# Kernel tuning notes

Measured on AMD Instinct MI355X. Metric: run time of the kernel, lower is better.

Reference implementation:

```python
import jax, jax.numpy as jnp
import numpy as np

T, H, NH, NKV, HD, E, K, I = 1024, 2048, 16, 4, 128, 16, 2, 768
EPS = 1e-6
THETA = 10000.0


def setup_inputs() -> dict:
    key = jax.random.key(0)
    ks = jax.random.split(key, 8)
    s = 0.02
    return {
        "hidden_states": jax.random.normal(ks[0], (T, H), jnp.float32),
        "positions": jnp.arange(T, dtype=jnp.int32),
        "w_norm1": jnp.ones((H,), jnp.float32),
        "w_norm2": jnp.ones((H,), jnp.float32),
        "w_qkv": jax.random.normal(ks[1], (H, (NH + 2 * NKV) * HD), jnp.float32) * s,
        "w_qnorm": jnp.ones((HD,), jnp.float32),
        "w_knorm": jnp.ones((HD,), jnp.float32),
        "w_o": jax.random.normal(ks[2], (NH * HD, H), jnp.float32) * s,
        "w_router": jax.random.normal(ks[3], (H, E), jnp.float32) * s,
        "w_gate": jax.random.normal(ks[4], (E, H, I), jnp.float32) * s,
        "w_up": jax.random.normal(ks[5], (E, H, I), jnp.float32) * s,
        "w_down": jax.random.normal(ks[6], (E, I, H), jnp.float32) * s,
    }


def rmsnorm(x, w):
    return x * jax.lax.rsqrt(jnp.mean(x * x, axis=-1, keepdims=True) + EPS) * w


def apply_rope(x, positions):
    # NEOX-style rotary, full head_dim. x: [T, n_heads, HD]
    half = HD // 2
    inv_freq = 1.0 / (THETA ** (jnp.arange(half, dtype=jnp.float32) / half))
    ang = positions.astype(jnp.float32)[:, None] * inv_freq  # [T, half]
    cos = jnp.cos(ang)[:, None, :]
    sin = jnp.sin(ang)[:, None, :]
    x1, x2 = x[..., :half], x[..., half:]
    return jnp.concatenate([x1 * cos - x2 * sin, x2 * cos + x1 * sin], axis=-1)


def reference(hidden_states, positions, w_norm1, w_norm2, w_qkv, w_qnorm, w_knorm,
              w_o, w_router, w_gate, w_up, w_down):
    # prepare_attn: residual = x; h = input_layernorm(x)
    residual = hidden_states
    h = rmsnorm(hidden_states, w_norm1)

    # --- attention (bidirectional, GQA, per-head q/k RMSNorm + RoPE) ---
    qkv = h @ w_qkv
    q, k, v = jnp.split(qkv, [NH * HD, NH * HD + NKV * HD], axis=-1)
    q = rmsnorm(q.reshape(T, NH, HD), w_qnorm)
    k = rmsnorm(k.reshape(T, NKV, HD), w_knorm)
    v = v.reshape(T, NKV, HD)
    q = apply_rope(q, positions)
    k = apply_rope(k, positions)
    rep = NH // NKV
    kf = jnp.repeat(k, rep, axis=1)  # [T, NH, HD]
    vf = jnp.repeat(v, rep, axis=1)
    scores = jnp.einsum('tnd,snd->nts', q, kf) * (HD ** -0.5)  # [NH, T, T]
    p = jax.nn.softmax(scores, axis=-1)
    ctx = jnp.einsum('nts,snd->tnd', p, vf).reshape(T, NH * HD)
    attn_out = ctx @ w_o

    # prepare_mlp: residual = residual + attn_out; h = post_attention_layernorm(residual)
    residual = residual + attn_out
    h = rmsnorm(residual, w_norm2)

    # --- sparse MoE: softmax router, top-k renormalize, SwiGLU experts ---
    logits = h @ w_router
    probs = jax.nn.softmax(logits, axis=-1)
    topw, topi = jax.lax.top_k(probs, K)
    topw = topw / jnp.sum(topw, axis=-1, keepdims=True)
    gates = jnp.zeros((T, E), h.dtype).at[jnp.arange(T)[:, None], topi].set(topw)
    g = jnp.einsum('th,ehi->eti', h, w_gate)
    u = jnp.einsum('th,ehi->eti', h, w_up)
    y = jnp.einsum('eti,eih->eth', jax.nn.silu(g) * u, w_down)
    moe_out = jnp.einsum('eth,te->th', y, gates)

    return moe_out, residual
```

## Files before the change

kernel.cpp:

```cpp
#include <hip/hip_runtime.h>

#define T_    1024
#define H_    2048
#define NH_   16
#define NKV_  4
#define HD_   128
#define E_    16
#define I_    768
#define QKVN  3072

typedef __attribute__((ext_vector_type(8))) short  short8;
typedef __attribute__((ext_vector_type(4))) float  f32x4;
typedef unsigned short u16;

#define LDP 40

__device__ inline u16 f2bf(float f) {
  unsigned u = __builtin_bit_cast(unsigned, f);
  return (u16)((u + 0x7fffu + ((u >> 16) & 1u)) >> 16);
}
__device__ inline float bf2f(u16 h) {
  unsigned u = ((unsigned)h) << 16;
  return __builtin_bit_cast(float, u);
}

__device__ inline float blk_sum(float v, float* lds) {
#pragma unroll
  for (int o = 32; o; o >>= 1) v += __shfl_down(v, o);
  int w = threadIdx.x >> 6;
  __syncthreads();
  if ((threadIdx.x & 63) == 0) lds[w] = v;
  __syncthreads();
  float s = lds[0];
  int nw = blockDim.x >> 6;
  for (int i = 1; i < nw; ++i) s += lds[i];
  return s;
}
__device__ inline float blk_max(float v, float* lds) {
#pragma unroll
  for (int o = 32; o; o >>= 1) v = fmaxf(v, __shfl_down(v, o));
  int w = threadIdx.x >> 6;
  __syncthreads();
  if ((threadIdx.x & 63) == 0) lds[w] = v;
  __syncthreads();
  float s = lds[0];
  int nw = blockDim.x >> 6;
  for (int i = 1; i < nw; ++i) s = fmaxf(s, lds[i]);
  return s;
}


struct F8 { float v[8]; };

__device__ inline void wrS(u16* lds, const uint4& r) {
  int row = threadIdx.x >> 2, kg = (threadIdx.x & 3) * 8;
  *(uint4*)(lds + row * LDP + kg) = r;
}
__device__ inline void wrS(u16* lds, const F8& r) {
  int n = threadIdx.x & 127, kh = (threadIdx.x >> 7) * 8;
  uint4 w;
  w.x = (unsigned)f2bf(r.v[0]) | ((unsigned)f2bf(r.v[1]) << 16);
  w.y = (unsigned)f2bf(r.v[2]) | ((unsigned)f2bf(r.v[3]) << 16);
  w.z = (unsigned)f2bf(r.v[4]) | ((unsigned)f2bf(r.v[5]) << 16);
  w.w = (unsigned)f2bf(r.v[6]) | ((unsigned)f2bf(r.v[7]) << 16);
  *(uint4*)(lds + n * LDP + kh) = w;
}

__device__ inline void mma8(const u16* As, const u16* Bs, f32x4 acc[4][2]) {
  const int lane = threadIdx.x & 63, wv = threadIdx.x >> 6;
  const int wr = wv >> 2, wc = wv & 3;
  const int kk = (lane >> 4) * 8, rr = lane & 15;
  short8 aF[4], bF[2];
#pragma unroll
  for (int m = 0; m < 4; ++m)
    aF[m] = *(const short8*)(As + (wr * 64 + m * 16 + rr) * LDP + kk);
#pragma unroll
  for (int n = 0; n < 2; ++n)
    bF[n] = *(const short8*)(Bs + (wc * 32 + n * 16 + rr) * LDP + kk);
#pragma unroll
  for (int m = 0; m < 4; ++m)
#pragma unroll
    for (int n = 0; n < 2; ++n)
      acc[m][n] = __builtin_amdgcn_mfma_f32_16x16x32_bf16(aF[m], bF[n], acc[m][n], 0, 0, 0);
}

#define ZERO_ACC(acc) do { \
  _Pragma("unroll") for (int m_ = 0; m_ < 4; ++m_) \
  _Pragma("unroll") for (int n_ = 0; n_ < 2; ++n_) acc[m_][n_] = (f32x4){0.f,0.f,0.f,0.f}; \
} while (0)

#define EPI_ROW(m, r)  (((threadIdx.x >> 6) >> 2) * 64 + (m)*16 + (((threadIdx.x&63) >> 4) * 4) + (r))
#define EPI_COL(n)     ((((threadIdx.x >> 6) & 3) * 32) + (n)*16 + ((threadIdx.x&63) & 15))

template<int NT, class BT, class LA, class LB>
__device__ inline void pipe(LA la, LB lb, u16* A0, u16* B0, u16* A1, u16* B1,
                            f32x4 acc[4][2]) {
  uint4 a0, a1; BT b0, b1;
  la(a0, 0); lb(b0, 0);
  la(a1, 1); lb(b1, 1);
  wrS(A0, a0); wrS(B0, b0);
  la(a0, 2); lb(b0, 2);
#pragma unroll 1
  for (int kt = 0; kt < NT; kt += 2) {
    __syncthreads();
    wrS(A1, a1); wrS(B1, b1);
    if (kt + 3 < NT) { la(a1, kt + 3); lb(b1, kt + 3); }
    mma8(A0, B0, acc);
    __syncthreads();
    if (kt + 2 < NT) { wrS(A0, a0); wrS(B0, b0); }
    if (kt + 4 < NT) { la(a0, kt + 4); lb(b0, kt + 4); }
    mma8(A1, B1, acc);
  }
}


__global__ __launch_bounds__(256) void k_rms1(const float* x, const float* w, u16* out) {
  __shared__ float lds[4];
  int t = blockIdx.x, tid = threadIdx.x;
  float v[8]; float ss = 0.f;
#pragma unroll
  for (int i = 0; i < 8; ++i) { v[i] = x[(size_t)t * H_ + tid + 256 * i]; ss += v[i] * v[i]; }
  ss = blk_sum(ss, lds);
  float inv = rsqrtf(ss * (1.f / H_) + 1e-6f);
#pragma unroll
  for (int i = 0; i < 8; ++i)
    out[(size_t)t * H_ + tid + 256 * i] = f2bf(v[i] * inv * w[tid + 256 * i]);
}

__global__ __launch_bounds__(256) void k_rms2(const float* x, const float* w,
                                              float* outf, u16* outb) {
  __shared__ float lds[4];
  int t = blockIdx.x, tid = threadIdx.x;
  float v[8]; float ss = 0.f;
#pragma unroll
  for (int i = 0; i < 8; ++i) { v[i] = x[(size_t)t * H_ + tid + 256 * i]; ss += v[i] * v[i]; }
  ss = blk_sum(ss, lds);
  float inv = rsqrtf(ss * (1.f / H_) + 1e-6f);
#pragma unroll
  for (int i = 0; i < 8; ++i) {
    float r = v[i] * inv * w[tid + 256 * i];
    outf[(size_t)t * H_ + tid + 256 * i] = r;
    outb[(size_t)t * H_ + tid + 256 * i] = f2bf(r);
  }
}

__global__ __launch_bounds__(512) void k_qkv(const u16* h1, const float* wqkv, float* qkv) {
  __shared__ __align__(16) u16 A0[128 * LDP], B0[128 * LDP], A1[128 * LDP], B1[128 * LDP];
  int bn = blockIdx.x, bm = blockIdx.y;
  f32x4 acc[4][2]; ZERO_ACC(acc);
  auto la = [&](uint4& r, int kt) {
    int row = threadIdx.x >> 2, kg = (threadIdx.x & 3) * 8;
    r = *(const uint4*)(h1 + (size_t)(bm * 128 + row) * H_ + kt * 32 + kg);
  };
  auto lb = [&](F8& r, int kt) {
    int n = threadIdx.x & 127, kh = (threadIdx.x >> 7) * 8;
    const float* src = wqkv + (size_t)(kt * 32 + kh) * QKVN + bn * 128 + n;
#pragma unroll
    for (int j = 0; j < 8; ++j) r.v[j] = src[(size_t)j * QKVN];
  };
  pipe<H_ / 32, F8>(la, lb, A0, B0, A1, B1, acc);
#pragma unroll
  for (int m = 0; m < 4; ++m)
#pragma unroll
    for (int n = 0; n < 2; ++n) {
      f32x4 a = acc[m][n];
#pragma unroll
      for (int r = 0; r < 4; ++r)
        qkv[(size_t)(bm * 128 + EPI_ROW(m, r)) * QKVN + bn * 128 + EPI_COL(n)] = a[r];
    }
}

__global__ __launch_bounds__(256) void k_qkrope(const float* qkv, const int* pos,
                                                const float* wq, const float* wk,
                                                u16* q, u16* kk, u16* vT) {
  __shared__ float cs[64], sn[64];
  int t = blockIdx.x, tid = threadIdx.x, lane = tid & 63, w = tid >> 6;
  if (tid < 64) {
    float fr = expf(-((float)tid / 64.f) * 9.210340371976184f);
    float ang = (float)pos[t] * fr;
    float s_, c_; sincosf(ang, &s_, &c_);
    cs[tid] = c_; sn[tid] = s_;
  }
  __syncthreads();
  const float* row = qkv + (size_t)t * QKVN;
  for (int h = w; h < NH_; h += 4) {
    float x1 = row[h * 128 + lane], x2 = row[h * 128 + 64 + lane];
    float ss = x1 * x1 + x2 * x2;
#pragma unroll
    for (int o = 32; o; o >>= 1) ss += __shfl_down(ss, o);
    ss = __shfl(ss, 0);
    float inv = rsqrtf(ss * (1.f / HD_) + 1e-6f);
    float n1 = x1 * inv * wq[lane], n2 = x2 * inv * wq[64 + lane];
    float o1 = n1 * cs[lane] - n2 * sn[lane];
    float o2 = n2 * cs[lane] + n1 * sn[lane];
    q[(size_t)t * (NH_ * HD_) + h * 128 + lane] = f2bf(o1);
    q[(size_t)t * (NH_ * HD_) + h * 128 + 64 + lane] = f2bf(o2);
  }
  if (w < NKV_) {
    int h = w;
    float x1 = row[2048 + h * 128 + lane], x2 = row[2048 + h * 128 + 64 + lane];
    float ss = x1 * x1 + x2 * x2;
#pragma unroll
    for (int o = 32; o; o >>= 1) ss += __shfl_down(ss, o);
    ss = __shfl(ss, 0);
    float inv = rsqrtf(ss * (1.f / HD_) + 1e-6f);
    float n1 = x1 * inv * wk[lane], n2 = x2 * inv * wk[64 + lane];
    float o1 = n1 * cs[lane] - n2 * sn[lane];
    float o2 = n2 * cs[lane] + n1 * sn[lane];
    kk[((size_t)h * T_ + t) * HD_ + lane] = f2bf(o1);
    kk[((size_t)h * T_ + t) * HD_ + 64 + lane] = f2bf(o2);
    float v1 = row[2560 + h * 128 + lane], v2 = row[2560 + h * 128 + 64 + lane];
    vT[((size_t)(h * 128 + lane)) * T_ + t] = f2bf(v1);
    vT[((size_t)(h * 128 + 64 + lane)) * T_ + t] = f2bf(v2);
  }
}

__global__ __launch_bounds__(512) void k_scores(const u16* q, const u16* kb, u16* S) {
  __shared__ __align__(16) u16 A0[128 * LDP], B0[128 * LDP], A1[128 * LDP], B1[128 * LDP];
  int h = blockIdx.x, sn = blockIdx.y, qm = blockIdx.z;
  const u16* Aq = q + h * 128;
  const u16* Bk = kb + (size_t)(h >> 2) * T_ * HD_;
  f32x4 acc[4][2]; ZERO_ACC(acc);
  auto la = [&](uint4& r, int kt) {
    int row = threadIdx.x >> 2, kg = (threadIdx.x & 3) * 8;
    r = *(const uint4*)(Aq + (size_t)(qm * 128 + row) * (NH_ * HD_) + kt * 32 + kg);
  };
  auto lb = [&](uint4& r, int kt) {
    int row = threadIdx.x >> 2, kg = (threadIdx.x & 3) * 8;
    r = *(const uint4*)(Bk + (size_t)(sn * 128 + row) * HD_ + kt * 32 + kg);
  };
  pipe<HD_ / 32, uint4>(la, lb, A0, B0, A1, B1, acc);
  const float scale = 0.08838834764831845f;
#pragma unroll
  for (int m = 0; m < 4; ++m)
#pragma unroll
    for (int n = 0; n < 2; ++n) {
      f32x4 a = acc[m][n];
#pragma unroll
      for (int r = 0; r < 4; ++r)
        S[((size_t)h * T_ + qm * 128 + EPI_ROW(m, r)) * T_ + sn * 128 + EPI_COL(n)] =
            f2bf(a[r] * scale);
    }
}

__global__ __launch_bounds__(256) void k_softmax(u16* S) {
  __shared__ float lds[4];
  int t = blockIdx.x, h = blockIdx.y, tid = threadIdx.x;
  u16* rowp = S + ((size_t)h * T_ + t) * T_;
  float x[4];
#pragma unroll
  for (int i = 0; i < 4; ++i) x[i] = bf2f(rowp[tid + 256 * i]);
  float m = fmaxf(fmaxf(x[0], x[1]), fmaxf(x[2], x[3]));
  m = blk_max(m, lds);
  float s = 0.f;
#pragma unroll
  for (int i = 0; i < 4; ++i) { x[i] = __expf(x[i] - m); s += x[i]; }
  s = blk_sum(s, lds);
  float inv = 1.f / s;
#pragma unroll
  for (int i = 0; i < 4; ++i) rowp[tid + 256 * i] = f2bf(x[i] * inv);
}

__global__ __launch_bounds__(512) void k_pv(const u16* P, const u16* vT, u16* ctx) {
  __shared__ __align__(16) u16 A0[128 * LDP], B0[128 * LDP], A1[128 * LDP], B1[128 * LDP];
  int h = blockIdx.x, qm = blockIdx.y;
  const u16* Ap = P + (size_t)h * T_ * T_;
  const u16* Bv = vT + (size_t)(h >> 2) * HD_ * T_;
  f32x4 acc[4][2]; ZERO_ACC(acc);
  auto la = [&](uint4& r, int kt) {
    int row = threadIdx.x >> 2, kg = (threadIdx.x & 3) * 8;
    r = *(const uint4*)(Ap + (size_t)(qm * 128 + row) * T_ + kt * 32 + kg);
  };
  auto lb = [&](uint4& r, int kt) {
    int row = threadIdx.x >> 2, kg = (threadIdx.x & 3) * 8;
    r = *(const uint4*)(Bv + (size_t)row * T_ + kt * 32 + kg);
  };
  pipe<T_ / 32, uint4>(la, lb, A0, B0, A1, B1, acc);
#pragma unroll
  for (int m = 0; m < 4; ++m)
#pragma unroll
    for (int n = 0; n < 2; ++n) {
      f32x4 a = acc[m][n];
#pragma unroll
      for (int r = 0; r < 4; ++r)
        ctx[(size_t)(qm * 128 + EPI_ROW(m, r)) * (NH_ * HD_) + h * 128 + EPI_COL(n)] =
            f2bf(a[r]);
    }
}

__global__ __launch_bounds__(512) void k_wo(const u16* ctx, const float* wo,
                                            const float* hs, float* resid) {
  __shared__ __align__(16) u16 A0[128 * LDP], B0[128 * LDP], A1[128 * LDP], B1[128 * LDP];
  int bn = blockIdx.x, bm = blockIdx.y;
  f32x4 acc[4][2]; ZERO_ACC(acc);
  auto la = [&](uint4& r, int kt) {
    int row = threadIdx.x >> 2, kg = (threadIdx.x & 3) * 8;
    r = *(const uint4*)(ctx + (size_t)(bm * 128 + row) * H_ + kt * 32 + kg);
  };
  auto lb = [&](F8& r, int kt) {
    int n = threadIdx.x & 127, kh = (threadIdx.x >> 7) * 8;
    const float* src = wo + (size_t)(kt * 32 + kh) * H_ + bn * 128 + n;
#pragma unroll
    for (int j = 0; j < 8; ++j) r.v[j] = src[(size_t)j * H_];
  };
  pipe<H_ / 32, F8>(la, lb, A0, B0, A1, B1, acc);
#pragma unroll
  for (int m = 0; m < 4; ++m)
#pragma unroll
    for (int n = 0; n < 2; ++n) {
      f32x4 a = acc[m][n];
#pragma unroll
      for (int r = 0; r < 4; ++r) {
        size_t idx = (size_t)(bm * 128 + EPI_ROW(m, r)) * H_ + bn * 128 + EPI_COL(n);
        resid[idx] = a[r] + hs[idx];
      }
    }
}

__global__ __launch_bounds__(256) void k_router(const float* h2f, const float* wr_,
                                                int* topi, float* topw, int* cnt) {
  __shared__ float xs[H_];
  __shared__ float red[4][16];
  __shared__ float lg[16];
  int t = blockIdx.x, tid = threadIdx.x;
#pragma unroll
  for (int i = 0; i < 8; ++i) xs[tid + 256 * i] = h2f[(size_t)t * H_ + tid + 256 * i];
  __syncthreads();
  int e = tid & 15, p = tid >> 4;
  float s = 0.f;
  int b0 = p * 128;
  for (int i = 0; i < 128; ++i) s += xs[b0 + i] * wr_[(size_t)(b0 + i) * E_ + e];
  s += __shfl_down(s, 32);
  s += __shfl_down(s, 16);
  int lane = tid & 63, w = tid >> 6;
  if (lane < 16) red[w][lane] = s;
  __syncthreads();
  if (tid < 16) lg[tid] = red[0][tid] + red[1][tid] + red[2][tid] + red[3][tid];
  __syncthreads();
  if (tid == 0) {
    float l1 = -1e30f; int e1 = 0;
    for (int i = 0; i < E_; ++i) if (lg[i] > l1) { l1 = lg[i]; e1 = i; }
    float l2 = -1e30f; int e2 = 0;
    for (int i = 0; i < E_; ++i) if (i != e1 && lg[i] > l2) { l2 = lg[i]; e2 = i; }
    float d = __expf(l2 - l1);
    float w1 = 1.f / (1.f + d), w2 = d / (1.f + d);
    topi[2 * t] = e1; topi[2 * t + 1] = e2;
    topw[2 * t] = w1; topw[2 * t + 1] = w2;
    atomicAdd(&cnt[e1], 1);
    atomicAdd(&cnt[e2], 1);
  }
}

__global__ void k_scan(const int* cnt, int* basearr) {
  if (threadIdx.x == 0) {
    int b = 0;
    for (int e = 0; e < E_; ++e) { basearr[e] = b; b += cnt[e]; }
    basearr[E_] = b;
  }
}

__global__ __launch_bounds__(256) void k_assign(const int* topi, const float* topw,
                                                const int* basearr, int* posc,
                                                int* tok, float* wslot) {
  int t = blockIdx.x * 256 + threadIdx.x;
  if (t < T_) {
#pragma unroll
    for (int j = 0; j < 2; ++j) {
      int e = topi[2 * t + j];
      int p = atomicAdd(&posc[e], 1);
      int s = basearr[e] + p;
      tok[s] = t;
      wslot[s] = topw[2 * t + j];
    }
  }
}

__global__ __launch_bounds__(512) void k_gateup(const u16* h2b,
                                                const float* wg, const float* wu,
                                                const int* cnt, const int* basearr, const int* tok,
                                                u16* act) {
  __shared__ __align__(16) u16 A0[128 * LDP], B0[128 * LDP], A1[128 * LDP], B1[128 * LDP];
  __shared__ int gat_s[128];
  int e = blockIdx.x;
  int c = cnt[e];
  int mt = blockIdx.z;
  if (mt * 128 >= c) return;
  int basee = basearr[e];
  int gmax = c - mt * 128;
  int n0 = blockIdx.y * 64;
  int tid = threadIdx.x;
  if (tid < 128) {
    int r = mt * 128 + tid;
    gat_s[tid] = (r < c) ? tok[basee + r] : tok[basee];
  }
  __syncthreads();
  const float* Bg = wg + (size_t)e * H_ * I_;
  const float* Bu = wu + (size_t)e * H_ * I_;
  f32x4 acc[4][2]; ZERO_ACC(acc);
  auto la = [&](uint4& r, int kt) {
    int row = threadIdx.x >> 2, kg = (threadIdx.x & 3) * 8;
    r = *(const uint4*)(h2b + (size_t)gat_s[row] * H_ + kt * 32 + kg);
  };
  auto lb = [&](F8& r, int kt) {
    int cidx = threadIdx.x & 127, kh = (threadIdx.x >> 7) * 8;
    int fn = cidx >> 4;
    const float* base = (fn & 1) ? Bu : Bg;
    int col = n0 + (fn >> 1) * 16 + (cidx & 15);
    const float* src = base + (size_t)(kt * 32 + kh) * I_ + col;
#pragma unroll
    for (int j = 0; j < 8; ++j) r.v[j] = src[(size_t)j * I_];
  };
  pipe<H_ / 32, F8>(la, lb, A0, B0, A1, B1, acc);
  int slot0 = basee + mt * 128;
#pragma unroll
  for (int m = 0; m < 4; ++m) {
#pragma unroll
    for (int r = 0; r < 4; ++r) {
      int row = EPI_ROW(m, r);
      if (row >= gmax) continue;
      int col = n0 + ((threadIdx.x >> 6) & 3) * 16 + ((threadIdx.x & 63) & 15);
      float g = acc[m][0][r], u = acc[m][1][r];
      float sg = g / (1.f + __expf(-g));
      act[(size_t)(slot0 + row) * I_ + col] = f2bf(sg * u);
    }
  }
}

__global__ __launch_bounds__(512) void k_down(const u16* act, const float* wd,
                                              const int* cnt, const int* basearr,
                                              const int* tok, const float* wslot,
                                              float* moe) {
  __shared__ __align__(16) u16 A0[128 * LDP], B0[128 * LDP], A1[128 * LDP], B1[128 * LDP];
  int e = blockIdx.y;
  int c = cnt[e];
  int mt = blockIdx.z;
  if (mt * 128 >= c) return;
  int basee = basearr[e];
  int gmax = c - mt * 128;
  int slot0 = basee + mt * 128;
  int n0 = blockIdx.x * 128;
  const u16* Ap = act + (size_t)slot0 * I_;
  const float* Bp = wd + (size_t)e * I_ * H_;
  f32x4 acc[4][2]; ZERO_ACC(acc);
  auto la = [&](uint4& r, int kt) {
    int row = threadIdx.x >> 2, kg = (threadIdx.x & 3) * 8;
    r = *(const uint4*)(Ap + (size_t)row * I_ + kt * 32 + kg);
  };
  auto lb = [&](F8& r, int kt) {
    int n = threadIdx.x & 127, kh = (threadIdx.x >> 7) * 8;
    const float* src = Bp + (size_t)(kt * 32 + kh) * H_ + n0 + n;
#pragma unroll
    for (int j = 0; j < 8; ++j) r.v[j] = src[(size_t)j * H_];
  };
  pipe<I_ / 32, F8>(la, lb, A0, B0, A1, B1, acc);
#pragma unroll
  for (int m = 0; m < 4; ++m)
#pragma unroll
    for (int n = 0; n < 2; ++n) {
      f32x4 a = acc[m][n];
#pragma unroll
      for (int r = 0; r < 4; ++r) {
        int row = EPI_ROW(m, r);
        if (row >= gmax) continue;
        int col = EPI_COL(n);
        int slot = slot0 + row;
        float wgt = wslot[slot];
        int tk = tok[slot];
        atomicAdd(&moe[(size_t)tk * H_ + n0 + col], a[r] * wgt);
      }
    }
}

extern "C" void kernel_launch(void* const* d_in, const int* in_sizes, int n_in,
                              void* d_out, int out_size, void* d_ws, size_t ws_size,
                              hipStream_t stream) {
  const float* hs    = (const float*)d_in[0];
  const int*   pos   = (const int*)d_in[1];
  const float* wn1   = (const float*)d_in[2];
  const float* wn2   = (const float*)d_in[3];
  const float* wqkv  = (const float*)d_in[4];
  const float* wqn   = (const float*)d_in[5];
  const float* wkn   = (const float*)d_in[6];
  const float* wo    = (const float*)d_in[7];
  const float* wrt   = (const float*)d_in[8];
  const float* wg    = (const float*)d_in[9];
  const float* wu    = (const float*)d_in[10];
  const float* wd    = (const float*)d_in[11];
  float* out = (float*)d_out;
  float* moe_out = out;
  float* resid   = out + (size_t)T_ * H_;

  char* ws = (char*)d_ws;
  size_t off = 0;
  auto alloc = [&](size_t bytes) { size_t r = off; off = (off + bytes + 255) & ~(size_t)255; return r; };
  u16*   h1   = (u16*)  (ws + alloc((size_t)T_ * H_ * 2));
  float* qkv  = (float*)(ws + alloc((size_t)T_ * QKVN * 4));
  u16*   q    = (u16*)  (ws + alloc((size_t)T_ * NH_ * HD_ * 2));
  u16*   kb   = (u16*)  (ws + alloc((size_t)NKV_ * T_ * HD_ * 2));
  u16*   vT   = (u16*)  (ws + alloc((size_t)NKV_ * HD_ * T_ * 2));
  u16*   S    = (u16*)  (ws + alloc((size_t)NH_ * T_ * T_ * 2));
  u16*   ctx  = (u16*)  (ws + alloc((size_t)T_ * NH_ * HD_ * 2));
  float* h2f  = (float*)(ws + alloc((size_t)T_ * H_ * 4));
  u16*   h2b  = (u16*)  (ws + alloc((size_t)T_ * H_ * 2));
  u16*   act  = (u16*)  (ws + alloc((size_t)(2 * T_ + 256) * I_ * 2));
  int*   topi = (int*)  (ws + alloc((size_t)T_ * 2 * 4));
  float* topw = (float*)(ws + alloc((size_t)T_ * 2 * 4));
  int*   cnt  = (int*)  (ws + alloc(32 * 4));
  int*   posc = cnt + 16;
  int*   base = (int*)  (ws + alloc(32 * 4));
  int*   tok  = (int*)  (ws + alloc((size_t)(2 * T_ + 128) * 4));
  float* wsl  = (float*)(ws + alloc((size_t)(2 * T_ + 128) * 4));
  (void)ws_size; (void)in_sizes; (void)n_in; (void)out_size;

  hipMemsetAsync(moe_out, 0, (size_t)T_ * H_ * 4, stream);
  hipMemsetAsync(cnt, 0, 32 * 4, stream);

  k_rms1<<<T_, 256, 0, stream>>>(hs, wn1, h1);
  k_qkv<<<dim3(QKVN / 128, T_ / 128), 512, 0, stream>>>(h1, wqkv, qkv);
  k_qkrope<<<T_, 256, 0, stream>>>(qkv, pos, wqn, wkn, q, kb, vT);
  k_scores<<<dim3(NH_, T_ / 128, T_ / 128), 512, 0, stream>>>(q, kb, S);
  k_softmax<<<dim3(T_, NH_), 256, 0, stream>>>(S);
  k_pv<<<dim3(NH_, T_ / 128), 512, 0, stream>>>(S, vT, ctx);
  k_wo<<<dim3(H_ / 128, T_ / 128), 512, 0, stream>>>(ctx, wo, hs, resid);
  k_rms2<<<T_, 256, 0, stream>>>(resid, wn2, h2f, h2b);
  k_router<<<T_, 256, 0, stream>>>(h2f, wrt, topi, topw, cnt);
  k_scan<<<1, 64, 0, stream>>>(cnt, base);
  k_assign<<<4, 256, 0, stream>>>(topi, topw, base, posc, tok, wsl);
  k_gateup<<<dim3(E_, I_ / 64, T_ / 128), 512, 0, stream>>>(h2b, wg, wu, cnt, base, tok, act);
  k_down<<<dim3(H_ / 128, E_, T_ / 128), 512, 0, stream>>>(act, wd, cnt, base, tok, wsl, moe_out);
}
```

Measured before the change: 353.1 us.

## Shrink GEMM tiles to 128x64 with 4-wave blocks and deeper register prefetch

All MFMA GEMM kernels move from 128x128 tiles with 8 waves to 128x64 tiles with 4 waves, doubling grid sizes, and k_pv gains a head-dim split. The A tile load becomes two uint4 per thread. The pipeline now keeps four k-steps of global loads in registers, up from two. This is meant to raise block count and occupancy for these small GEMMs and hide more load latency, at the cost of more register pressure and lower per-block data reuse (more redundant A-tile reads).

```diff
diff --git a/kernel.cpp b/kernel.cpp
--- a/kernel.cpp
+++ b/kernel.cpp
@@ -50,14 +50,19 @@
 }
 
 
+struct A2 { uint4 x, y; };
 struct F8 { float v[8]; };
 
+__device__ inline void wrS(u16* lds, const A2& r) {
+  int u0 = threadIdx.x, u1 = threadIdx.x + 256;
+  *(uint4*)(lds + (u0 >> 2) * LDP + (u0 & 3) * 8) = r.x;
+  *(uint4*)(lds + (u1 >> 2) * LDP + (u1 & 3) * 8) = r.y;
+}
 __device__ inline void wrS(u16* lds, const uint4& r) {
-  int row = threadIdx.x >> 2, kg = (threadIdx.x & 3) * 8;
-  *(uint4*)(lds + row * LDP + kg) = r;
+  *(uint4*)(lds + (threadIdx.x >> 2) * LDP + (threadIdx.x & 3) * 8) = r;
 }
 __device__ inline void wrS(u16* lds, const F8& r) {
-  int n = threadIdx.x & 127, kh = (threadIdx.x >> 7) * 8;
+  int n = threadIdx.x & 63, kh = (threadIdx.x >> 6) * 8;
   uint4 w;
   w.x = (unsigned)f2bf(r.v[0]) | ((unsigned)f2bf(r.v[1]) << 16);
   w.y = (unsigned)f2bf(r.v[2]) | ((unsigned)f2bf(r.v[3]) << 16);
@@ -66,9 +71,9 @@
   *(uint4*)(lds + n * LDP + kh) = w;
 }
 
-__device__ inline void mma8(const u16* As, const u16* Bs, f32x4 acc[4][2]) {
+__device__ inline void mma4(const u16* As, const u16* Bs, f32x4 acc[4][2]) {
   const int lane = threadIdx.x & 63, wv = threadIdx.x >> 6;
-  const int wr = wv >> 2, wc = wv & 3;
+  const int wr = wv >> 1, wc = wv & 1;
   const int kk = (lane >> 4) * 8, rr = lane & 15;
   short8 aF[4], bF[2];
 #pragma unroll
@@ -89,27 +94,35 @@
   _Pragma("unroll") for (int n_ = 0; n_ < 2; ++n_) acc[m_][n_] = (f32x4){0.f,0.f,0.f,0.f}; \
 } while (0)
 
-#define EPI_ROW(m, r)  (((threadIdx.x >> 6) >> 2) * 64 + (m)*16 + (((threadIdx.x&63) >> 4) * 4) + (r))
-#define EPI_COL(n)     ((((threadIdx.x >> 6) & 3) * 32) + (n)*16 + ((threadIdx.x&63) & 15))
-
-template<int NT, class BT, class LA, class LB>
-__device__ inline void pipe(LA la, LB lb, u16* A0, u16* B0, u16* A1, u16* B1,
-                            f32x4 acc[4][2]) {
-  uint4 a0, a1; BT b0, b1;
-  la(a0, 0); lb(b0, 0);
-  la(a1, 1); lb(b1, 1);
+#define EPI_ROW(m, r)  (((threadIdx.x >> 6) >> 1) * 64 + (m)*16 + (((threadIdx.x&63) >> 4) * 4) + (r))
+#define EPI_COL(n)     ((((threadIdx.x >> 6) & 1) * 32) + (n)*16 + ((threadIdx.x&63) & 15))
+
+template<int NT, class AT, class BT, class LA, class LB>
+__device__ inline void pipe4(LA la, LB lb, u16* A0, u16* B0, u16* A1, u16* B1,
+                             f32x4 acc[4][2]) {
+  AT a0, a1, a2, a3; BT b0, b1, b2, b3;
+  la(a0, 0); lb(b0, 0); la(a1, 1); lb(b1, 1);
+  la(a2, 2); lb(b2, 2); la(a3, 3); lb(b3, 3);
   wrS(A0, a0); wrS(B0, b0);
-  la(a0, 2); lb(b0, 2);
+  if (NT > 4) { la(a0, 4); lb(b0, 4); }
 #pragma unroll 1
-  for (int kt = 0; kt < NT; kt += 2) {
+  for (int kt = 0; kt < NT; kt += 4) {
     __syncthreads();
     wrS(A1, a1); wrS(B1, b1);
-    if (kt + 3 < NT) { la(a1, kt + 3); lb(b1, kt + 3); }
-    mma8(A0, B0, acc);
+    if (kt + 5 < NT) { la(a1, kt + 5); lb(b1, kt + 5); }
+    mma4(A0, B0, acc);
     __syncthreads();
-    if (kt + 2 < NT) { wrS(A0, a0); wrS(B0, b0); }
-    if (kt + 4 < NT) { la(a0, kt + 4); lb(b0, kt + 4); }
-    mma8(A1, B1, acc);
+    wrS(A0, a2); wrS(B0, b2);
+    if (kt + 6 < NT) { la(a2, kt + 6); lb(b2, kt + 6); }
+    mma4(A1, B1, acc);
+    __syncthreads();
+    wrS(A1, a3); wrS(B1, b3);
+    if (kt + 7 < NT) { la(a3, kt + 7); lb(b3, kt + 7); }
+    mma4(A0, B0, acc);
+    __syncthreads();
+    if (kt + 4 < NT) { wrS(A0, a0); wrS(B0, b0); }
+    if (kt + 8 < NT) { la(a0, kt + 8); lb(b0, kt + 8); }
+    mma4(A1, B1, acc);
   }
 }
 
@@ -144,21 +157,22 @@
   }
 }
 
-__global__ __launch_bounds__(512) void k_qkv(const u16* h1, const float* wqkv, float* qkv) {
-  __shared__ __align__(16) u16 A0[128 * LDP], B0[128 * LDP], A1[128 * LDP], B1[128 * LDP];
+__global__ __launch_bounds__(256) void k_qkv(const u16* h1, const float* wqkv, float* qkv) {
+  __shared__ __align__(16) u16 A0[128 * LDP], B0[64 * LDP], A1[128 * LDP], B1[64 * LDP];
   int bn = blockIdx.x, bm = blockIdx.y;
   f32x4 acc[4][2]; ZERO_ACC(acc);
-  auto la = [&](uint4& r, int kt) {
-    int row = threadIdx.x >> 2, kg = (threadIdx.x & 3) * 8;
-    r = *(const uint4*)(h1 + (size_t)(bm * 128 + row) * H_ + kt * 32 + kg);
+  auto la = [&](A2& r, int kt) {
+    int u0 = threadIdx.x, u1 = threadIdx.x + 256;
+    r.x = *(const uint4*)(h1 + (size_t)(bm * 128 + (u0 >> 2)) * H_ + kt * 32 + (u0 & 3) * 8);
+    r.y = *(const uint4*)(h1 + (size_t)(bm * 128 + (u1 >> 2)) * H_ + kt * 32 + (u1 & 3) * 8);
   };
   auto lb = [&](F8& r, int kt) {
-    int n = threadIdx.x & 127, kh = (threadIdx.x >> 7) * 8;
-    const float* src = wqkv + (size_t)(kt * 32 + kh) * QKVN + bn * 128 + n;
+    int n = threadIdx.x & 63, kh = (threadIdx.x >> 6) * 8;
+    const float* src = wqkv + (size_t)(kt * 32 + kh) * QKVN + bn * 64 + n;
 #pragma unroll
     for (int j = 0; j < 8; ++j) r.v[j] = src[(size_t)j * QKVN];
   };
-  pipe<H_ / 32, F8>(la, lb, A0, B0, A1, B1, acc);
+  pipe4<H_ / 32, A2, F8>(la, lb, A0, B0, A1, B1, acc);
 #pragma unroll
   for (int m = 0; m < 4; ++m)
 #pragma unroll
@@ -166,7 +180,7 @@
       f32x4 a = acc[m][n];
 #pragma unroll
       for (int r = 0; r < 4; ++r)
-        qkv[(size_t)(bm * 128 + EPI_ROW(m, r)) * QKVN + bn * 128 + EPI_COL(n)] = a[r];
+        qkv[(size_t)(bm * 128 + EPI_ROW(m, r)) * QKVN + bn * 64 + EPI_COL(n)] = a[r];
     }
 }
 
@@ -215,21 +229,21 @@
   }
 }
 
-__global__ __launch_bounds__(512) void k_scores(const u16* q, const u16* kb, u16* S) {
-  __shared__ __align__(16) u16 A0[128 * LDP], B0[128 * LDP], A1[128 * LDP], B1[128 * LDP];
+__global__ __launch_bounds__(256) void k_scores(const u16* q, const u16* kb, u16* S) {
+  __shared__ __align__(16) u16 A0[128 * LDP], B0[64 * LDP], A1[128 * LDP], B1[64 * LDP];
   int h = blockIdx.x, sn = blockIdx.y, qm = blockIdx.z;
   const u16* Aq = q + h * 128;
   const u16* Bk = kb + (size_t)(h >> 2) * T_ * HD_;
   f32x4 acc[4][2]; ZERO_ACC(acc);
-  auto la = [&](uint4& r, int kt) {
-    int row = threadIdx.x >> 2, kg = (threadIdx.x & 3) * 8;
-    r = *(const uint4*)(Aq + (size_t)(qm * 128 + row) * (NH_ * HD_) + kt * 32 + kg);
+  auto la = [&](A2& r, int kt) {
+    int u0 = threadIdx.x, u1 = threadIdx.x + 256;
+    r.x = *(const uint4*)(Aq + (size_t)(qm * 128 + (u0 >> 2)) * (NH_ * HD_) + kt * 32 + (u0 & 3) * 8);
+    r.y = *(const uint4*)(Aq + (size_t)(qm * 128 + (u1 >> 2)) * (NH_ * HD_) + kt * 32 + (u1 & 3) * 8);
   };
   auto lb = [&](uint4& r, int kt) {
-    int row = threadIdx.x >> 2, kg = (threadIdx.x & 3) * 8;
-    r = *(const uint4*)(Bk + (size_t)(sn * 128 + row) * HD_ + kt * 32 + kg);
-  };
-  pipe<HD_ / 32, uint4>(la, lb, A0, B0, A1, B1, acc);
+    r = *(const uint4*)(Bk + (size_t)(sn * 64 + (threadIdx.x >> 2)) * HD_ + kt * 32 + (threadIdx.x & 3) * 8);
+  };
+  pipe4<HD_ / 32, A2, uint4>(la, lb, A0, B0, A1, B1, acc);
   const float scale = 0.08838834764831845f;
 #pragma unroll
   for (int m = 0; m < 4; ++m)
@@ -238,7 +252,7 @@
       f32x4 a = acc[m][n];
 #pragma unroll
       for (int r = 0; r < 4; ++r)
-        S[((size_t)h * T_ + qm * 128 + EPI_ROW(m, r)) * T_ + sn * 128 + EPI_COL(n)] =
+        S[((size_t)h * T_ + qm * 128 + EPI_ROW(m, r)) * T_ + sn * 64 + EPI_COL(n)] =
             f2bf(a[r] * scale);
     }
 }
@@ -261,21 +275,21 @@
   for (int i = 0; i < 4; ++i) rowp[tid + 256 * i] = f2bf(x[i] * inv);
 }
 
-__global__ __launch_bounds__(512) void k_pv(const u16* P, const u16* vT, u16* ctx) {
-  __shared__ __align__(16) u16 A0[128 * LDP], B0[128 * LDP], A1[128 * LDP], B1[128 * LDP];
-  int h = blockIdx.x, qm = blockIdx.y;
+__global__ __launch_bounds__(256) void k_pv(const u16* P, const u16* vT, u16* ctx) {
+  __shared__ __align__(16) u16 A0[128 * LDP], B0[64 * LDP], A1[128 * LDP], B1[64 * LDP];
+  int h = blockIdx.x, qm = blockIdx.y, nb = blockIdx.z;
   const u16* Ap = P + (size_t)h * T_ * T_;
-  const u16* Bv = vT + (size_t)(h >> 2) * HD_ * T_;
+  const u16* Bv = vT + (size_t)(h >> 2) * HD_ * T_ + (size_t)nb * 64 * T_;
   f32x4 acc[4][2]; ZERO_ACC(acc);
-  auto la = [&](uint4& r, int kt) {
-    int row = threadIdx.x >> 2, kg = (threadIdx.x & 3) * 8;
-    r = *(const uint4*)(Ap + (size_t)(qm * 128 + row) * T_ + kt * 32 + kg);
+  auto la = [&](A2& r, int kt) {
+    int u0 = threadIdx.x, u1 = threadIdx.x + 256;
+    r.x = *(const uint4*)(Ap + (size_t)(qm * 128 + (u0 >> 2)) * T_ + kt * 32 + (u0 & 3) * 8);
+    r.y = *(const uint4*)(Ap + (size_t)(qm * 128 + (u1 >> 2)) * T_ + kt * 32 + (u1 & 3) * 8);
   };
   auto lb = [&](uint4& r, int kt) {
-    int row = threadIdx.x >> 2, kg = (threadIdx.x & 3) * 8;
-    r = *(const uint4*)(Bv + (size_t)row * T_ + kt * 32 + kg);
-  };
-  pipe<T_ / 32, uint4>(la, lb, A0, B0, A1, B1, acc);
+    r = *(const uint4*)(Bv + (size_t)(threadIdx.x >> 2) * T_ + kt * 32 + (threadIdx.x & 3) * 8);
+  };
+  pipe4<T_ / 32, A2, uint4>(la, lb, A0, B0, A1, B1, acc);
 #pragma unroll
   for (int m = 0; m < 4; ++m)
 #pragma unroll
@@ -283,27 +297,28 @@
       f32x4 a = acc[m][n];
 #pragma unroll
       for (int r = 0; r < 4; ++r)
-        ctx[(size_t)(qm * 128 + EPI_ROW(m, r)) * (NH_ * HD_) + h * 128 + EPI_COL(n)] =
+        ctx[(size_t)(qm * 128 + EPI_ROW(m, r)) * (NH_ * HD_) + h * 128 + nb * 64 + EPI_COL(n)] =
             f2bf(a[r]);
     }
 }
 
-__global__ __launch_bounds__(512) void k_wo(const u16* ctx, const float* wo,
+__global__ __launch_bounds__(256) void k_wo(const u16* ctx, const float* wo,
                                             const float* hs, float* resid) {
-  __shared__ __align__(16) u16 A0[128 * LDP], B0[128 * LDP], A1[128 * LDP], B1[128 * LDP];
+  __shared__ __align__(16) u16 A0[128 * LDP], B0[64 * LDP], A1[128 * LDP], B1[64 * LDP];
   int bn = blockIdx.x, bm = blockIdx.y;
   f32x4 acc[4][2]; ZERO_ACC(acc);
-  auto la = [&](uint4& r, int kt) {
-    int row = threadIdx.x >> 2, kg = (threadIdx.x & 3) * 8;
-    r = *(const uint4*)(ctx + (size_t)(bm * 128 + row) * H_ + kt * 32 + kg);
+  auto la = [&](A2& r, int kt) {
+    int u0 = threadIdx.x, u1 = threadIdx.x + 256;
+    r.x = *(const uint4*)(ctx + (size_t)(bm * 128 + (u0 >> 2)) * H_ + kt * 32 + (u0 & 3) * 8);
+    r.y = *(const uint4*)(ctx + (size_t)(bm * 128 + (u1 >> 2)) * H_ + kt * 32 + (u1 & 3) * 8);
   };
   auto lb = [&](F8& r, int kt) {
-    int n = threadIdx.x & 127, kh = (threadIdx.x >> 7) * 8;
-    const float* src = wo + (size_t)(kt * 32 + kh) * H_ + bn * 128 + n;
+    int n = threadIdx.x & 63, kh = (threadIdx.x >> 6) * 8;
+    const float* src = wo + (size_t)(kt * 32 + kh) * H_ + bn * 64 + n;
 #pragma unroll
     for (int j = 0; j < 8; ++j) r.v[j] = src[(size_t)j * H_];
   };
-  pipe<H_ / 32, F8>(la, lb, A0, B0, A1, B1, acc);
+  pipe4<H_ / 32, A2, F8>(la, lb, A0, B0, A1, B1, acc);
 #pragma unroll
   for (int m = 0; m < 4; ++m)
 #pragma unroll
@@ -311,7 +326,7 @@
       f32x4 a = acc[m][n];
 #pragma unroll
       for (int r = 0; r < 4; ++r) {
-        size_t idx = (size_t)(bm * 128 + EPI_ROW(m, r)) * H_ + bn * 128 + EPI_COL(n);
+        size_t idx = (size_t)(bm * 128 + EPI_ROW(m, r)) * H_ + bn * 64 + EPI_COL(n);
         resid[idx] = a[r] + hs[idx];
       }
     }
@@ -375,11 +390,11 @@
   }
 }
 
-__global__ __launch_bounds__(512) void k_gateup(const u16* h2b,
+__global__ __launch_bounds__(256) void k_gateup(const u16* h2b,
                                                 const float* wg, const float* wu,
                                                 const int* cnt, const int* basearr, const int* tok,
                                                 u16* act) {
-  __shared__ __align__(16) u16 A0[128 * LDP], B0[128 * LDP], A1[128 * LDP], B1[128 * LDP];
+  __shared__ __align__(16) u16 A0[128 * LDP], B0[64 * LDP], A1[128 * LDP], B1[64 * LDP];
   __shared__ int gat_s[128];
   int e = blockIdx.x;
   int c = cnt[e];
@@ -387,7 +402,7 @@
   if (mt * 128 >= c) return;
   int basee = basearr[e];
   int gmax = c - mt * 128;
-  int n0 = blockIdx.y * 64;
+  int n0 = blockIdx.y * 32;
   int tid = threadIdx.x;
   if (tid < 128) {
     int r = mt * 128 + tid;
@@ -397,12 +412,13 @@
   const float* Bg = wg + (size_t)e * H_ * I_;
   const float* Bu = wu + (size_t)e * H_ * I_;
   f32x4 acc[4][2]; ZERO_ACC(acc);
-  auto la = [&](uint4& r, int kt) {
-    int row = threadIdx.x >> 2, kg = (threadIdx.x & 3) * 8;
-    r = *(const uint4*)(h2b + (size_t)gat_s[row] * H_ + kt * 32 + kg);
+  auto la = [&](A2& r, int kt) {
+    int u0 = threadIdx.x, u1 = threadIdx.x + 256;
+    r.x = *(const uint4*)(h2b + (size_t)gat_s[u0 >> 2] * H_ + kt * 32 + (u0 & 3) * 8);
+    r.y = *(const uint4*)(h2b + (size_t)gat_s[u1 >> 2] * H_ + kt * 32 + (u1 & 3) * 8);
   };
   auto lb = [&](F8& r, int kt) {
-    int cidx = threadIdx.x & 127, kh = (threadIdx.x >> 7) * 8;
+    int cidx = threadIdx.x & 63, kh = (threadIdx.x >> 6) * 8;
     int fn = cidx >> 4;
     const float* base = (fn & 1) ? Bu : Bg;
     int col = n0 + (fn >> 1) * 16 + (cidx & 15);
@@ -410,15 +426,15 @@
 #pragma unroll
     for (int j = 0; j < 8; ++j) r.v[j] = src[(size_t)j * I_];
   };
-  pipe<H_ / 32, F8>(la, lb, A0, B0, A1, B1, acc);
+  pipe4<H_ / 32, A2, F8>(la, lb, A0, B0, A1, B1, acc);
   int slot0 = basee + mt * 128;
+  int col = n0 + ((threadIdx.x >> 6) & 1) * 16 + ((threadIdx.x & 63) & 15);
 #pragma unroll
   for (int m = 0; m < 4; ++m) {
 #pragma unroll
     for (int r = 0; r < 4; ++r) {
       int row = EPI_ROW(m, r);
       if (row >= gmax) continue;
-      int col = n0 + ((threadIdx.x >> 6) & 3) * 16 + ((threadIdx.x & 63) & 15);
       float g = acc[m][0][r], u = acc[m][1][r];
       float sg = g / (1.f + __expf(-g));
       act[(size_t)(slot0 + row) * I_ + col] = f2bf(sg * u);
@@ -426,11 +442,11 @@
   }
 }
 
-__global__ __launch_bounds__(512) void k_down(const u16* act, const float* wd,
+__global__ __launch_bounds__(256) void k_down(const u16* act, const float* wd,
                                               const int* cnt, const int* basearr,
                                               const int* tok, const float* wslot,
                                               float* moe) {
-  __shared__ __align__(16) u16 A0[128 * LDP], B0[128 * LDP], A1[128 * LDP], B1[128 * LDP];
+  __shared__ __align__(16) u16 A0[128 * LDP], B0[64 * LDP], A1[128 * LDP], B1[64 * LDP];
   int e = blockIdx.y;
   int c = cnt[e];
   int mt = blockIdx.z;
@@ -438,21 +454,22 @@
   int basee = basearr[e];
   int gmax = c - mt * 128;
   int slot0 = basee + mt * 128;
-  int n0 = blockIdx.x * 128;
+  int n0 = blockIdx.x * 64;
   const u16* Ap = act + (size_t)slot0 * I_;
   const float* Bp = wd + (size_t)e * I_ * H_;
   f32x4 acc[4][2]; ZERO_ACC(acc);
-  auto la = [&](uint4& r, int kt) {
-    int row = threadIdx.x >> 2, kg = (threadIdx.x & 3) * 8;
-    r = *(const uint4*)(Ap + (size_t)row * I_ + kt * 32 + kg);
+  auto la = [&](A2& r, int kt) {
+    int u0 = threadIdx.x, u1 = threadIdx.x + 256;
+    r.x = *(const uint4*)(Ap + (size_t)(u0 >> 2) * I_ + kt * 32 + (u0 & 3) * 8);
+    r.y = *(const uint4*)(Ap + (size_t)(u1 >> 2) * I_ + kt * 32 + (u1 & 3) * 8);
   };
   auto lb = [&](F8& r, int kt) {
-    int n = threadIdx.x & 127, kh = (threadIdx.x >> 7) * 8;
+    int n = threadIdx.x & 63, kh = (threadIdx.x >> 6) * 8;
     const float* src = Bp + (size_t)(kt * 32 + kh) * H_ + n0 + n;
 #pragma unroll
     for (int j = 0; j < 8; ++j) r.v[j] = src[(size_t)j * H_];
   };
-  pipe<I_ / 32, F8>(la, lb, A0, B0, A1, B1, acc);
+  pipe4<I_ / 32, A2, F8>(la, lb, A0, B0, A1, B1, acc);
 #pragma unroll
   for (int m = 0; m < 4; ++m)
 #pragma unroll
@@ -516,16 +533,16 @@
   hipMemsetAsync(cnt, 0, 32 * 4, stream);
 
   k_rms1<<<T_, 256, 0, stream>>>(hs, wn1, h1);
-  k_qkv<<<dim3(QKVN / 128, T_ / 128), 512, 0, stream>>>(h1, wqkv, qkv);
+  k_qkv<<<dim3(QKVN / 64, T_ / 128), 256, 0, stream>>>(h1, wqkv, qkv);
   k_qkrope<<<T_, 256, 0, stream>>>(qkv, pos, wqn, wkn, q, kb, vT);
-  k_scores<<<dim3(NH_, T_ / 128, T_ / 128), 512, 0, stream>>>(q, kb, S);
+  k_scores<<<dim3(NH_, T_ / 64, T_ / 128), 256, 0, stream>>>(q, kb, S);
   k_softmax<<<dim3(T_, NH_), 256, 0, stream>>>(S);
-  k_pv<<<dim3(NH_, T_ / 128), 512, 0, stream>>>(S, vT, ctx);
-  k_wo<<<dim3(H_ / 128, T_ / 128), 512, 0, stream>>>(ctx, wo, hs, resid);
+  k_pv<<<dim3(NH_, T_ / 128, HD_ / 64), 256, 0, stream>>>(S, vT, ctx);
+  k_wo<<<dim3(H_ / 64, T_ / 128), 256, 0, stream>>>(ctx, wo, hs, resid);
   k_rms2<<<T_, 256, 0, stream>>>(resid, wn2, h2f, h2b);
   k_router<<<T_, 256, 0, stream>>>(h2f, wrt, topi, topw, cnt);
   k_scan<<<1, 64, 0, stream>>>(cnt, base);
   k_assign<<<4, 256, 0, stream>>>(topi, topw, base, posc, tok, wsl);
-  k_gateup<<<dim3(E_, I_ / 64, T_ / 128), 512, 0, stream>>>(h2b, wg, wu, cnt, base, tok, act);
-  k_down<<<dim3(H_ / 128, E_, T_ / 128), 512, 0, stream>>>(act, wd, cnt, base, tok, wsl, moe_out);
-}
+  k_gateup<<<dim3(E_, I_ / 32, T_ / 128), 256, 0, stream>>>(h2b, wg, wu, cnt, base, tok, act);
+  k_down<<<dim3(H_ / 64, E_, T_ / 128), 256, 0, stream>>>(act, wd, cnt, base, tok, wsl, moe_out);
+}
```

Result: slower. 593.5 us (+68.1%).
